# Kernel optimization log

Hardware: AMD Instinct MI355X
Metric: run time of the kernel (lower is better)

The kernel has to match this reference:

```python
import jax, jax.numpy as jnp
import numpy as np

VTH = 1.0
U_REST = -VTH          # default u_rest = -vth
DV = VTH - U_REST      # reset-subtract magnitude = 2.0
LEAKY = 0.9
FB_NUM = 1

B, D_IN, N, L, T = 16384, 512, 512, 3, 32
W_SCALE = 0.05


def _lif(u):
    # threshold-compare, reset-subtract, leaky-decay
    s = (u >= VTH).astype(u.dtype)
    u = (u - DV * s) * LEAKY
    return u, s


def setup_inputs() -> dict:
    key = jax.random.key(0)
    k1, k2, k3 = jax.random.split(key, 3)
    x = jax.random.normal(k1, (B, D_IN), dtype=jnp.float32)
    Wx = jax.random.normal(k2, (N, D_IN), dtype=jnp.float32) * W_SCALE
    bx = jnp.zeros((N,), dtype=jnp.float32)
    Ws = jax.random.normal(k3, (L, N, N), dtype=jnp.float32) * W_SCALE
    bs = jnp.zeros((L, N), dtype=jnp.float32)
    return {"x": x, "Wx": Wx, "bx": bx, "Ws": Ws, "bs": bs, "time_step": T}


def reference(x, Wx, bx, Ws, bs, time_step):
    L_ = Ws.shape[0]
    x1 = x @ Wx.T + bx  # constant input current, [B, N]

    # ---- first timestep: initialize all layers sequentially ----
    u0, s0 = _lif(x1)
    us, ss = [u0], [s0]
    for i in range(L_ - 1):
        ui, si = _lif(ss[-1] @ Ws[i].T + bs[i])
        us.append(ui)
        ss.append(si)
    u = jnp.stack(us)  # [L, B, N]
    s = jnp.stack(ss)
    a = s              # leaky-weighted spike accumulator

    # ---- remaining time_step-1 steps ----
    def step(carry, _):
        u, s, a = carry
        new_u, new_s = [], []
        # first layer gets feedback from last layer's spikes + constant input
        u0 = u[0] + s[L_ - 1] @ Ws[L_ - 1].T + bs[L_ - 1] + x1
        u0n, s0n = _lif(u0)
        new_u.append(u0n)
        new_s.append(s0n)
        # subsequent layers use the spikes just produced this timestep
        for i in range(L_ - 1):
            ui = u[i + 1] + new_s[i] @ Ws[i].T + bs[i]
            uin, sin_ = _lif(ui)
            new_u.append(uin)
            new_s.append(sin_)
        u = jnp.stack(new_u)
        s = jnp.stack(new_s)
        a = a * LEAKY + s
        return (u, s, a), None

    (u, s, a), _ = jax.lax.scan(step, (u, s, a), None, length=time_step - 1)

    weighted = (1.0 - LEAKY ** time_step) / (1.0 - LEAKY)
    a = a / weighted
    # f_type='all', fb_num=1 -> (a_list[0], a_list[-1])
    return a[0], a[L_ - 1]
```

## Files before the change

### kernel.cpp

```cpp
#include <hip/hip_runtime.h>
#include <stdint.h>


#define B_SZ 16384
#define N_SZ 512
#define K_SZ 512
#define T_STEPS 32
#define LEAKY 0.9f

#define CHUNK 16

__device__ inline uint32_t spread4(uint32_t b) {
    b = (b | (b << 12)) & 0x000F000Fu;
    b = (b | (b << 6))  & 0x03030303u;
    b = (b | (b << 3))  & 0x11111111u;
    return b;
}

__device__ inline uint32_t mask_word8(const unsigned long long bal[8], int lane) {
    const uint32_t sh = (4u * (uint32_t)lane) & 31u;
    uint32_t word = 0;
    #pragma unroll
    for (int j = 0; j < 8; ++j) {
        const uint32_t half = (lane < 8) ? (uint32_t)bal[j] : (uint32_t)(bal[j] >> 32);
        const uint32_t nib  = (half >> sh) & 0xFu;
        word |= ((nib * 0x00204081u) & 0x01010101u) << j;
    }
    return word;
}

template<int AMODE, bool ADD_U, bool ADD_X1>
__global__ __launch_bounds__(1024, 1)
void spgemm_lif(const uint32_t* __restrict__ mIn,
                const float* __restrict__ Wt,
                const float* __restrict__ bias,
                const float* u_prev,
                const float* __restrict__ x1,
                float* u_out,
                uint32_t* __restrict__ mOut,
                float* a_ptr)
{
    __shared__ float Wl[2][CHUNK * 512];

    const int tid  = threadIdx.x;
    const int lane = tid & 63;
    const int w    = tid >> 6;
    const int rg   = w >> 1;
    const int g    = w & 1;
    const int r0   = blockIdx.x * 64 + rg * 8;
    const int cb   = g * 256 + lane * 4;

    float acc[8][4];
    #pragma unroll
    for (int m = 0; m < 8; ++m)
        #pragma unroll
        for (int j = 0; j < 4; ++j) acc[m][j] = 0.f;

    auto stage = [&](int c, int bf) {
        const float* src = Wt + (size_t)c * (CHUNK * 512);
        #pragma unroll
        for (int i = 0; i < 2; ++i) {
            const int seg = w * 2 + i;
            __builtin_amdgcn_global_load_lds(
                (const __attribute__((address_space(1))) unsigned int*)
                    (src + seg * 256 + lane * 4),
                (__attribute__((address_space(3))) unsigned int*)
                    (&Wl[bf][seg * 256]),
                16, 0, 0);
        }
    };

    auto compute = [&](int bf, const uint32_t* msr, int sh) {
        const float* base = &Wl[bf][0];
        #pragma unroll
        for (int m = 0; m < 8; ++m) {
            uint32_t wrd = (msr[m] >> sh) & 0xFFFFu;
            while (wrd) {
                const int kk = __builtin_ctz(wrd);
                wrd &= wrd - 1u;
                const float4 wv = *(const float4*)(base + kk * 512 + cb);
                acc[m][0] += wv.x;
                acc[m][1] += wv.y;
                acc[m][2] += wv.z;
                acc[m][3] += wv.w;
            }
        }
    };

    uint32_t mv = mIn[r0 + (lane & 7)];
    stage(0, 0);
    __syncthreads();

    int cur = 0;
    uint32_t msr[8];
    for (int c = 0; c < 32; ++c) {
        if (c + 1 < 32) stage(c + 1, cur ^ 1);
        if ((c & 1) == 0) {
            #pragma unroll
            for (int m = 0; m < 8; ++m)
                msr[m] = __builtin_amdgcn_readlane(mv, m);
            const int pn = (c >> 1) + 1;
            if (pn < 16) mv = mIn[(size_t)pn * B_SZ + r0 + (lane & 7)];
        }
        compute(cur, msr, (c & 1) * 16);
        __syncthreads();
        cur ^= 1;
    }

    const float4 bv = *(const float4*)(bias + cb);
    const int msel = lane & 7;
    unsigned long long balsel[4] = {0ull, 0ull, 0ull, 0ull};

    #pragma unroll
    for (int m = 0; m < 8; ++m) {
        const size_t row = (size_t)(r0 + m) * N_SZ + cb;
        float v[4];
        v[0] = acc[m][0] + bv.x; v[1] = acc[m][1] + bv.y;
        v[2] = acc[m][2] + bv.z; v[3] = acc[m][3] + bv.w;
        if (ADD_U) {
            const float4 ua = *(const float4*)(u_prev + row);
            v[0] += ua.x; v[1] += ua.y; v[2] += ua.z; v[3] += ua.w;
        }
        if (ADD_X1) {
            const float4 xa = *(const float4*)(x1 + row);
            v[0] += xa.x; v[1] += xa.y; v[2] += xa.z; v[3] += xa.w;
        }
        float un[4], sv[4];
        #pragma unroll
        for (int j = 0; j < 4; ++j) {
            sv[j] = (v[j] >= 1.0f) ? 1.0f : 0.0f;
            un[j] = (v[j] - 2.0f * sv[j]) * LEAKY;
        }
        *(float4*)(u_out + row) = (float4){un[0], un[1], un[2], un[3]};
        if (AMODE == 1) {
            *(float4*)(a_ptr + row) = (float4){sv[0], sv[1], sv[2], sv[3]};
        } else if (AMODE == 2) {
            const float4 aa = *(const float4*)(a_ptr + row);
            *(float4*)(a_ptr + row) = (float4){aa.x * LEAKY + sv[0], aa.y * LEAKY + sv[1],
                                               aa.z * LEAKY + sv[2], aa.w * LEAKY + sv[3]};
        }
        unsigned long long bal[4];
        #pragma unroll
        for (int j = 0; j < 4; ++j) bal[j] = __ballot(v[j] >= 1.0f);
        #pragma unroll
        for (int j = 0; j < 4; ++j)
            balsel[j] = (m == msel) ? bal[j] : balsel[j];
    }

    const int h = lane >> 3;
    uint32_t pk = 0;
    #pragma unroll
    for (int j = 0; j < 4; ++j)
        pk |= spread4((uint32_t)(balsel[j] >> (8 * h)) & 0xFFu) << j;
    mOut[(size_t)(g * 8 + h) * B_SZ + r0 + msel] = pk;
}

__global__ void mask_build(const uint16_t* __restrict__ s, uint32_t* __restrict__ mOut) {
    const int lane = threadIdx.x & 63;
    const int w    = threadIdx.x >> 6;
    const int r0   = blockIdx.x * 32 + w * 8;
    const int cb   = lane * 8;
    uint32_t pk[8];
    #pragma unroll
    for (int m = 0; m < 8; ++m) {
        const ushort4 sa = ((const ushort4*)(s + (size_t)(r0 + m) * N_SZ + cb))[0];
        const ushort4 sb = ((const ushort4*)(s + (size_t)(r0 + m) * N_SZ + cb))[1];
        const uint16_t sv[8] = {sa.x, sa.y, sa.z, sa.w, sb.x, sb.y, sb.z, sb.w};
        unsigned long long bal[8];
        #pragma unroll
        for (int j = 0; j < 8; ++j) bal[j] = __ballot(sv[j] != 0);
        pk[m] = mask_word8(bal, lane);
    }
    if (lane < 16) {
        uint32_t* mp = mOut + (size_t)lane * B_SZ + r0;
        ((uint4*)mp)[0] = (uint4){pk[0], pk[1], pk[2], pk[3]};
        ((uint4*)mp)[1] = (uint4){pk[4], pk[5], pk[6], pk[7]};
    }
}

#define BM 128
#define BN 128
#define BK 16
#define TM 8
#define TN 8
#define PAD 4

__global__ __launch_bounds__(256, 2)
void gemm0_lif(const float* __restrict__ A, const float* __restrict__ W,
               const float* __restrict__ bias, float* __restrict__ u_out,
               uint16_t* __restrict__ s_out, float* __restrict__ a_ptr,
               float* __restrict__ c_out) {
    __shared__ float As[BK][BM + PAD];
    __shared__ float Bs[BK][BN + PAD];
    const int tid = threadIdx.x;
    const int tx = tid & 15, ty = tid >> 4;
    const int m0 = blockIdx.y * BM, n0 = blockIdx.x * BN;
    float acc[TM][TN];
    #pragma unroll
    for (int i = 0; i < TM; ++i)
        #pragma unroll
        for (int j = 0; j < TN; ++j) acc[i][j] = 0.f;
    const int lr = tid >> 2, lc = (tid & 3) * 4;
    for (int k0 = 0; k0 < K_SZ; k0 += BK) {
        #pragma unroll
        for (int h = 0; h < 2; ++h) {
            const int r = lr + h * 64;
            const float4 v = *(const float4*)(A + (size_t)(m0 + r) * K_SZ + k0 + lc);
            As[lc + 0][r] = v.x; As[lc + 1][r] = v.y;
            As[lc + 2][r] = v.z; As[lc + 3][r] = v.w;
        }
        #pragma unroll
        for (int h = 0; h < 2; ++h) {
            const int r = lr + h * 64;
            const float4 v = *(const float4*)(W + (size_t)(n0 + r) * K_SZ + k0 + lc);
            Bs[lc + 0][r] = v.x; Bs[lc + 1][r] = v.y;
            Bs[lc + 2][r] = v.z; Bs[lc + 3][r] = v.w;
        }
        __syncthreads();
        #pragma unroll
        for (int kk = 0; kk < BK; ++kk) {
            float av[TM], bvv[TN];
            #pragma unroll
            for (int i = 0; i < TM; ++i) av[i] = As[kk][ty * TM + i];
            #pragma unroll
            for (int j = 0; j < TN; ++j) bvv[j] = Bs[kk][tx * TN + j];
            #pragma unroll
            for (int i = 0; i < TM; ++i)
                #pragma unroll
                for (int j = 0; j < TN; ++j)
                    acc[i][j] = fmaf(av[i], bvv[j], acc[i][j]);
        }
        __syncthreads();
    }
    #pragma unroll
    for (int i = 0; i < TM; ++i) {
        const size_t row = (size_t)(m0 + ty * TM + i) * N_SZ + n0 + tx * TN;
        #pragma unroll
        for (int j = 0; j < TN; ++j) {
            const float v = acc[i][j] + bias[n0 + tx * TN + j];
            c_out[row + j] = v;
            const float sv = (v >= 1.0f) ? 1.0f : 0.0f;
            u_out[row + j] = (v - 2.0f * sv) * LEAKY;
            s_out[row + j] = (v >= 1.0f) ? (uint16_t)0x3F80 : (uint16_t)0;
            a_ptr[row + j] = sv;
        }
    }
}

__global__ void transpose512(const float* __restrict__ in, float* __restrict__ out) {
    __shared__ float t[32][33];
    const int mat = blockIdx.z;
    const int bx = blockIdx.x * 32, by = blockIdx.y * 32;
    const int x = threadIdx.x & 31, yg = threadIdx.x >> 5;
    const float* I = in + (size_t)mat * N_SZ * K_SZ;
    float* O = out + (size_t)mat * N_SZ * K_SZ;
    #pragma unroll
    for (int i = 0; i < 4; ++i)
        t[yg * 4 + i][x] = I[(size_t)(by + yg * 4 + i) * 512 + bx + x];
    __syncthreads();
    #pragma unroll
    for (int i = 0; i < 4; ++i)
        O[(size_t)(bx + yg * 4 + i) * 512 + by + x] = t[x][yg * 4 + i];
}

__global__ void scale_kernel(float* __restrict__ p, float inv, int n4) {
    int i = blockIdx.x * blockDim.x + threadIdx.x;
    const int stride = gridDim.x * blockDim.x;
    for (; i < n4; i += stride) {
        float4 v = ((float4*)p)[i];
        v.x *= inv; v.y *= inv; v.z *= inv; v.w *= inv;
        ((float4*)p)[i] = v;
    }
}

extern "C" void kernel_launch(void* const* d_in, const int* in_sizes, int n_in,
                              void* d_out, int out_size, void* d_ws, size_t ws_size,
                              hipStream_t stream) {
    const float* x  = (const float*)d_in[0];
    const float* Wx = (const float*)d_in[1];
    const float* bx = (const float*)d_in[2];
    const float* Ws = (const float*)d_in[3];
    const float* bs = (const float*)d_in[4];

    const size_t BNt = (size_t)B_SZ * N_SZ;
    const size_t NK  = (size_t)N_SZ * K_SZ;
    const size_t MSZ = (size_t)16 * B_SZ;

    float*    u   = (float*)d_ws;
    float*    x1  = u + 3 * BNt;
    uint16_t* s0b = (uint16_t*)(x1 + BNt);
    float*    WsT = (float*)(s0b + BNt);
    uint32_t* mT  = (uint32_t*)(WsT + 3 * NK + 4096);
    uint32_t* mT0 = mT;
    uint32_t* mT1 = mT + MSZ;
    uint32_t* mT2 = mT + 2 * MSZ;

    float* a0 = (float*)d_out;
    float* a2 = a0 + BNt;
    float* u0 = u; float* u1 = u + BNt; float* u2 = u + 2 * BNt;

    dim3 blkS(1024);
    dim3 blk(256);
    dim3 gridV(N_SZ / BN, B_SZ / BM);
    dim3 gridS(B_SZ / 64);
    dim3 gridM(B_SZ / 32);
    dim3 gridT(16, 16, 3);

    transpose512<<<gridT, blk, 0, stream>>>(Ws, WsT);

    gemm0_lif<<<gridV, blk, 0, stream>>>(x, Wx, bx, u0, s0b, a0, x1);
    mask_build<<<gridM, blk, 0, stream>>>(s0b, mT0);
    spgemm_lif<0, false, false><<<gridS, blkS, 0, stream>>>(
        mT0, WsT, bs, nullptr, nullptr, u1, mT1, nullptr);
    spgemm_lif<1, false, false><<<gridS, blkS, 0, stream>>>(
        mT1, WsT + NK, bs + N_SZ, nullptr, nullptr, u2, mT2, a2);

    for (int t = 1; t < T_STEPS; ++t) {
        spgemm_lif<2, true, true><<<gridS, blkS, 0, stream>>>(
            mT2, WsT + 2 * NK, bs + 2 * N_SZ, u0, x1, u0, mT0, a0);
        spgemm_lif<0, true, false><<<gridS, blkS, 0, stream>>>(
            mT0, WsT, bs, u1, nullptr, u1, mT1, nullptr);
        spgemm_lif<2, true, false><<<gridS, blkS, 0, stream>>>(
            mT1, WsT + NK, bs + N_SZ, u2, nullptr, u2, mT2, a2);
    }

    double p = 1.0;
    for (int i = 0; i < T_STEPS; ++i) p *= 0.9;
    const float inv = (float)(1.0 / ((1.0 - p) / 0.1));
    scale_kernel<<<2048, blk, 0, stream>>>((float*)d_out, inv, (int)(2 * BNt / 4));
}
```

Measured before the change: 6.365 ms.

## Split spike GEMM block into sparse LDS waves and dense FMA waves

Each 64-row block now runs 12 waves instead of 16. Eight waves handle the first 32 rows with the existing sparse, mask-driven accumulation from double-buffered LDS weight chunks. Four waves handle the other 32 rows with a dense, branch-free FMA loop that reads weights straight from global memory. Launch bounds change to 768 threads with two blocks per CU, aiming to overlap LDS-bound and VALU-bound work and to raise occupancy. The risk is that the dense half does the full K work regardless of spike sparsity and is tied to the sparse waves through shared barriers, so it may end up limiting the block.

```diff
diff --git a/kernel.cpp b/kernel.cpp
--- a/kernel.cpp
+++ b/kernel.cpp
@@ -30,8 +30,8 @@
 }
 
 template<int AMODE, bool ADD_U, bool ADD_X1>
-__global__ __launch_bounds__(1024, 1)
-void spgemm_lif(const uint32_t* __restrict__ mIn,
+__global__ __launch_bounds__(768, 2)
+void hybrid_lif(const uint32_t* __restrict__ mIn,
                 const float* __restrict__ Wt,
                 const float* __restrict__ bias,
                 const float* u_prev,
@@ -45,114 +45,236 @@
     const int tid  = threadIdx.x;
     const int lane = tid & 63;
     const int w    = tid >> 6;
-    const int rg   = w >> 1;
-    const int g    = w & 1;
-    const int r0   = blockIdx.x * 64 + rg * 8;
-    const int cb   = g * 256 + lane * 4;
-
-    float acc[8][4];
-    #pragma unroll
-    for (int m = 0; m < 8; ++m)
-        #pragma unroll
-        for (int j = 0; j < 4; ++j) acc[m][j] = 0.f;
-
-    auto stage = [&](int c, int bf) {
-        const float* src = Wt + (size_t)c * (CHUNK * 512);
-        #pragma unroll
-        for (int i = 0; i < 2; ++i) {
-            const int seg = w * 2 + i;
-            __builtin_amdgcn_global_load_lds(
-                (const __attribute__((address_space(1))) unsigned int*)
-                    (src + seg * 256 + lane * 4),
-                (__attribute__((address_space(3))) unsigned int*)
-                    (&Wl[bf][seg * 256]),
-                16, 0, 0);
-        }
-    };
-
-    auto compute = [&](int bf, const uint32_t* msr, int sh) {
-        const float* base = &Wl[bf][0];
+
+    if (w < 8) {
+        const int rg = w >> 1;
+        const int g  = w & 1;
+        const int r0 = blockIdx.x * 64 + rg * 8;
+        const int cb = g * 256 + lane * 4;
+
+        float acc[8][4];
+        #pragma unroll
+        for (int m = 0; m < 8; ++m)
+            #pragma unroll
+            for (int j = 0; j < 4; ++j) acc[m][j] = 0.f;
+
+        auto stage = [&](int c, int bf) {
+            const float* src = Wt + (size_t)c * (CHUNK * 512);
+            #pragma unroll
+            for (int i = 0; i < 4; ++i) {
+                const int seg = w * 4 + i;
+                __builtin_amdgcn_global_load_lds(
+                    (const __attribute__((address_space(1))) unsigned int*)
+                        (src + seg * 256 + lane * 4),
+                    (__attribute__((address_space(3))) unsigned int*)
+                        (&Wl[bf][seg * 256]),
+                    16, 0, 0);
+            }
+        };
+
+        auto compute = [&](int bf, const uint32_t* msr, int sh) {
+            const float* base = &Wl[bf][0];
+            #pragma unroll
+            for (int m = 0; m < 8; ++m) {
+                uint32_t wrd = (msr[m] >> sh) & 0xFFFFu;
+                while (wrd) {
+                    const int kk = __builtin_ctz(wrd);
+                    wrd &= wrd - 1u;
+                    const float4 wv = *(const float4*)(base + kk * 512 + cb);
+                    acc[m][0] += wv.x;
+                    acc[m][1] += wv.y;
+                    acc[m][2] += wv.z;
+                    acc[m][3] += wv.w;
+                }
+            }
+        };
+
+        uint32_t mv = mIn[r0 + (lane & 7)];
+        stage(0, 0);
+        __syncthreads();
+
+        int cur = 0;
+        uint32_t msr[8];
+        for (int c = 0; c < 32; ++c) {
+            if (c + 1 < 32) stage(c + 1, cur ^ 1);
+            if ((c & 1) == 0) {
+                #pragma unroll
+                for (int m = 0; m < 8; ++m)
+                    msr[m] = __builtin_amdgcn_readlane(mv, m);
+                const int pn = (c >> 1) + 1;
+                if (pn < 16) mv = mIn[(size_t)pn * B_SZ + r0 + (lane & 7)];
+            }
+            compute(cur, msr, (c & 1) * 16);
+            __syncthreads();
+            cur ^= 1;
+        }
+
+        const float4 bv = *(const float4*)(bias + cb);
+        const int msel = lane & 7;
+        unsigned long long balsel[4] = {0ull, 0ull, 0ull, 0ull};
+
         #pragma unroll
         for (int m = 0; m < 8; ++m) {
-            uint32_t wrd = (msr[m] >> sh) & 0xFFFFu;
-            while (wrd) {
-                const int kk = __builtin_ctz(wrd);
-                wrd &= wrd - 1u;
-                const float4 wv = *(const float4*)(base + kk * 512 + cb);
-                acc[m][0] += wv.x;
-                acc[m][1] += wv.y;
-                acc[m][2] += wv.z;
-                acc[m][3] += wv.w;
-            }
-        }
-    };
-
-    uint32_t mv = mIn[r0 + (lane & 7)];
-    stage(0, 0);
-    __syncthreads();
-
-    int cur = 0;
-    uint32_t msr[8];
-    for (int c = 0; c < 32; ++c) {
-        if (c + 1 < 32) stage(c + 1, cur ^ 1);
-        if ((c & 1) == 0) {
-            #pragma unroll
-            for (int m = 0; m < 8; ++m)
-                msr[m] = __builtin_amdgcn_readlane(mv, m);
-            const int pn = (c >> 1) + 1;
-            if (pn < 16) mv = mIn[(size_t)pn * B_SZ + r0 + (lane & 7)];
-        }
-        compute(cur, msr, (c & 1) * 16);
+            const size_t row = (size_t)(r0 + m) * N_SZ + cb;
+            float v[4];
+            v[0] = acc[m][0] + bv.x; v[1] = acc[m][1] + bv.y;
+            v[2] = acc[m][2] + bv.z; v[3] = acc[m][3] + bv.w;
+            if (ADD_U) {
+                const float4 ua = *(const float4*)(u_prev + row);
+                v[0] += ua.x; v[1] += ua.y; v[2] += ua.z; v[3] += ua.w;
+            }
+            if (ADD_X1) {
+                const float4 xa = *(const float4*)(x1 + row);
+                v[0] += xa.x; v[1] += xa.y; v[2] += xa.z; v[3] += xa.w;
+            }
+            float un[4], sv[4];
+            #pragma unroll
+            for (int j = 0; j < 4; ++j) {
+                sv[j] = (v[j] >= 1.0f) ? 1.0f : 0.0f;
+                un[j] = (v[j] - 2.0f * sv[j]) * LEAKY;
+            }
+            *(float4*)(u_out + row) = (float4){un[0], un[1], un[2], un[3]};
+            if (AMODE == 1) {
+                *(float4*)(a_ptr + row) = (float4){sv[0], sv[1], sv[2], sv[3]};
+            } else if (AMODE == 2) {
+                const float4 aa = *(const float4*)(a_ptr + row);
+                *(float4*)(a_ptr + row) = (float4){aa.x * LEAKY + sv[0], aa.y * LEAKY + sv[1],
+                                                   aa.z * LEAKY + sv[2], aa.w * LEAKY + sv[3]};
+            }
+            unsigned long long bal[4];
+            #pragma unroll
+            for (int j = 0; j < 4; ++j) bal[j] = __ballot(v[j] >= 1.0f);
+            #pragma unroll
+            for (int j = 0; j < 4; ++j)
+                balsel[j] = (m == msel) ? bal[j] : balsel[j];
+        }
+
+        const int h = lane >> 3;
+        uint32_t pk = 0;
+        #pragma unroll
+        for (int j = 0; j < 4; ++j)
+            pk |= spread4((uint32_t)(balsel[j] >> (8 * h)) & 0xFFu) << j;
+        mOut[(size_t)(g * 8 + h) * B_SZ + r0 + msel] = pk;
+
+    } else {
+        const int r0 = blockIdx.x * 64 + 32 + (w - 8) * 8;
+        const int cb = lane * 8;
+
+        float acc[8][8];
+        #pragma unroll
+        for (int m = 0; m < 8; ++m)
+            #pragma unroll
+            for (int j = 0; j < 8; ++j) acc[m][j] = 0.f;
+
+        const float* wb = Wt + cb;
+        float4 w0a = ((const float4*)wb)[0];
+        float4 w0b = ((const float4*)wb)[1];
+        float4 w1a = ((const float4*)(wb + 512))[0];
+        float4 w1b = ((const float4*)(wb + 512))[1];
+
+        uint32_t mv = mIn[r0 + (lane & 7)];
         __syncthreads();
-        cur ^= 1;
-    }
-
-    const float4 bv = *(const float4*)(bias + cb);
-    const int msel = lane & 7;
-    unsigned long long balsel[4] = {0ull, 0ull, 0ull, 0ull};
-
-    #pragma unroll
-    for (int m = 0; m < 8; ++m) {
-        const size_t row = (size_t)(r0 + m) * N_SZ + cb;
-        float v[4];
-        v[0] = acc[m][0] + bv.x; v[1] = acc[m][1] + bv.y;
-        v[2] = acc[m][2] + bv.z; v[3] = acc[m][3] + bv.w;
-        if (ADD_U) {
-            const float4 ua = *(const float4*)(u_prev + row);
-            v[0] += ua.x; v[1] += ua.y; v[2] += ua.z; v[3] += ua.w;
-        }
-        if (ADD_X1) {
-            const float4 xa = *(const float4*)(x1 + row);
-            v[0] += xa.x; v[1] += xa.y; v[2] += xa.z; v[3] += xa.w;
-        }
-        float un[4], sv[4];
-        #pragma unroll
-        for (int j = 0; j < 4; ++j) {
-            sv[j] = (v[j] >= 1.0f) ? 1.0f : 0.0f;
-            un[j] = (v[j] - 2.0f * sv[j]) * LEAKY;
-        }
-        *(float4*)(u_out + row) = (float4){un[0], un[1], un[2], un[3]};
-        if (AMODE == 1) {
-            *(float4*)(a_ptr + row) = (float4){sv[0], sv[1], sv[2], sv[3]};
-        } else if (AMODE == 2) {
-            const float4 aa = *(const float4*)(a_ptr + row);
-            *(float4*)(a_ptr + row) = (float4){aa.x * LEAKY + sv[0], aa.y * LEAKY + sv[1],
-                                               aa.z * LEAKY + sv[2], aa.w * LEAKY + sv[3]};
-        }
-        unsigned long long bal[4];
-        #pragma unroll
-        for (int j = 0; j < 4; ++j) bal[j] = __ballot(v[j] >= 1.0f);
-        #pragma unroll
-        for (int j = 0; j < 4; ++j)
-            balsel[j] = (m == msel) ? bal[j] : balsel[j];
-    }
-
-    const int h = lane >> 3;
-    uint32_t pk = 0;
-    #pragma unroll
-    for (int j = 0; j < 4; ++j)
-        pk |= spread4((uint32_t)(balsel[j] >> (8 * h)) & 0xFFu) << j;
-    mOut[(size_t)(g * 8 + h) * B_SZ + r0 + msel] = pk;
+
+        uint32_t ms[8];
+        for (int c = 0; c < 32; ++c) {
+            if ((c & 1) == 0) {
+                #pragma unroll
+                for (int m = 0; m < 8; ++m)
+                    ms[m] = __builtin_amdgcn_readlane(mv, m);
+                const int pn = (c >> 1) + 1;
+                if (pn < 16) mv = mIn[(size_t)pn * B_SZ + r0 + (lane & 7)];
+            }
+            const int sh = (c & 1) * 16;
+            #pragma unroll
+            for (int kp = 0; kp < 8; ++kp) {
+                const int k = c * 16 + 2 * kp;
+                const float* pf = wb + (size_t)(k + 2) * 512;
+                const float4 n0a = ((const float4*)pf)[0];
+                const float4 n0b = ((const float4*)pf)[1];
+                const float4 n1a = ((const float4*)(pf + 512))[0];
+                const float4 n1b = ((const float4*)(pf + 512))[1];
+                #pragma unroll
+                for (int m = 0; m < 8; ++m) {
+                    const float sm = ((ms[m] >> (sh + 2 * kp)) & 1u) ? 1.0f : 0.0f;
+                    acc[m][0] = fmaf(sm, w0a.x, acc[m][0]);
+                    acc[m][1] = fmaf(sm, w0a.y, acc[m][1]);
+                    acc[m][2] = fmaf(sm, w0a.z, acc[m][2]);
+                    acc[m][3] = fmaf(sm, w0a.w, acc[m][3]);
+                    acc[m][4] = fmaf(sm, w0b.x, acc[m][4]);
+                    acc[m][5] = fmaf(sm, w0b.y, acc[m][5]);
+                    acc[m][6] = fmaf(sm, w0b.z, acc[m][6]);
+                    acc[m][7] = fmaf(sm, w0b.w, acc[m][7]);
+                }
+                #pragma unroll
+                for (int m = 0; m < 8; ++m) {
+                    const float sm = ((ms[m] >> (sh + 2 * kp + 1)) & 1u) ? 1.0f : 0.0f;
+                    acc[m][0] = fmaf(sm, w1a.x, acc[m][0]);
+                    acc[m][1] = fmaf(sm, w1a.y, acc[m][1]);
+                    acc[m][2] = fmaf(sm, w1a.z, acc[m][2]);
+                    acc[m][3] = fmaf(sm, w1a.w, acc[m][3]);
+                    acc[m][4] = fmaf(sm, w1b.x, acc[m][4]);
+                    acc[m][5] = fmaf(sm, w1b.y, acc[m][5]);
+                    acc[m][6] = fmaf(sm, w1b.z, acc[m][6]);
+                    acc[m][7] = fmaf(sm, w1b.w, acc[m][7]);
+                }
+                w0a = n0a; w0b = n0b; w1a = n1a; w1b = n1b;
+            }
+            __syncthreads();
+        }
+
+        float4 bva = ((const float4*)(bias + cb))[0];
+        float4 bvb = ((const float4*)(bias + cb))[1];
+        float bv[8] = {bva.x, bva.y, bva.z, bva.w, bvb.x, bvb.y, bvb.z, bvb.w};
+
+        uint32_t pk[8];
+        #pragma unroll
+        for (int m = 0; m < 8; ++m) {
+            const size_t row = (size_t)(r0 + m) * N_SZ + cb;
+            float v[8];
+            #pragma unroll
+            for (int j = 0; j < 8; ++j) v[j] = acc[m][j] + bv[j];
+            if (ADD_U) {
+                const float4 ua = ((const float4*)(u_prev + row))[0];
+                const float4 ub = ((const float4*)(u_prev + row))[1];
+                v[0] += ua.x; v[1] += ua.y; v[2] += ua.z; v[3] += ua.w;
+                v[4] += ub.x; v[5] += ub.y; v[6] += ub.z; v[7] += ub.w;
+            }
+            if (ADD_X1) {
+                const float4 xa = ((const float4*)(x1 + row))[0];
+                const float4 xb = ((const float4*)(x1 + row))[1];
+                v[0] += xa.x; v[1] += xa.y; v[2] += xa.z; v[3] += xa.w;
+                v[4] += xb.x; v[5] += xb.y; v[6] += xb.z; v[7] += xb.w;
+            }
+            float un[8], sv[8];
+            #pragma unroll
+            for (int j = 0; j < 8; ++j) {
+                sv[j] = (v[j] >= 1.0f) ? 1.0f : 0.0f;
+                un[j] = (v[j] - 2.0f * sv[j]) * LEAKY;
+            }
+            ((float4*)(u_out + row))[0] = (float4){un[0], un[1], un[2], un[3]};
+            ((float4*)(u_out + row))[1] = (float4){un[4], un[5], un[6], un[7]};
+            if (AMODE == 1) {
+                ((float4*)(a_ptr + row))[0] = (float4){sv[0], sv[1], sv[2], sv[3]};
+                ((float4*)(a_ptr + row))[1] = (float4){sv[4], sv[5], sv[6], sv[7]};
+            } else if (AMODE == 2) {
+                const float4 aa = ((const float4*)(a_ptr + row))[0];
+                const float4 ab = ((const float4*)(a_ptr + row))[1];
+                ((float4*)(a_ptr + row))[0] = (float4){aa.x * LEAKY + sv[0], aa.y * LEAKY + sv[1],
+                                                       aa.z * LEAKY + sv[2], aa.w * LEAKY + sv[3]};
+                ((float4*)(a_ptr + row))[1] = (float4){ab.x * LEAKY + sv[4], ab.y * LEAKY + sv[5],
+                                                       ab.z * LEAKY + sv[6], ab.w * LEAKY + sv[7]};
+            }
+            unsigned long long bal[8];
+            #pragma unroll
+            for (int j = 0; j < 8; ++j) bal[j] = __ballot(v[j] >= 1.0f);
+            pk[m] = mask_word8(bal, lane);
+        }
+        if (lane < 16) {
+            uint32_t* mp = mOut + (size_t)lane * B_SZ + r0;
+            ((uint4*)mp)[0] = (uint4){pk[0], pk[1], pk[2], pk[3]};
+            ((uint4*)mp)[1] = (uint4){pk[4], pk[5], pk[6], pk[7]};
+        }
+    }
 }
 
 __global__ void mask_build(const uint16_t* __restrict__ s, uint32_t* __restrict__ mOut) {
@@ -299,10 +421,10 @@
     float* a2 = a0 + BNt;
     float* u0 = u; float* u1 = u + BNt; float* u2 = u + 2 * BNt;
 
-    dim3 blkS(1024);
+    dim3 blkH(768);
     dim3 blk(256);
     dim3 gridV(N_SZ / BN, B_SZ / BM);
-    dim3 gridS(B_SZ / 64);
+    dim3 gridH(B_SZ / 64);
     dim3 gridM(B_SZ / 32);
     dim3 gridT(16, 16, 3);
 
@@ -310,17 +432,17 @@
 
     gemm0_lif<<<gridV, blk, 0, stream>>>(x, Wx, bx, u0, s0b, a0, x1);
     mask_build<<<gridM, blk, 0, stream>>>(s0b, mT0);
-    spgemm_lif<0, false, false><<<gridS, blkS, 0, stream>>>(
+    hybrid_lif<0, false, false><<<gridH, blkH, 0, stream>>>(
         mT0, WsT, bs, nullptr, nullptr, u1, mT1, nullptr);
-    spgemm_lif<1, false, false><<<gridS, blkS, 0, stream>>>(
+    hybrid_lif<1, false, false><<<gridH, blkH, 0, stream>>>(
         mT1, WsT + NK, bs + N_SZ, nullptr, nullptr, u2, mT2, a2);
 
     for (int t = 1; t < T_STEPS; ++t) {
-        spgemm_lif<2, true, true><<<gridS, blkS, 0, stream>>>(
+        hybrid_lif<2, true, true><<<gridH, blkH, 0, stream>>>(
             mT2, WsT + 2 * NK, bs + 2 * N_SZ, u0, x1, u0, mT0, a0);
-        spgemm_lif<0, true, false><<<gridS, blkS, 0, stream>>>(
+        hybrid_lif<0, true, false><<<gridH, blkH, 0, stream>>>(
             mT0, WsT, bs, u1, nullptr, u1, mT1, nullptr);
-        spgemm_lif<2, true, false><<<gridS, blkS, 0, stream>>>(
+        hybrid_lif<2, true, false><<<gridH, blkH, 0, stream>>>(
             mT1, WsT + NK, bs + N_SZ, u2, nullptr, u2, mT2, a2);
     }
 
```

Measured after the change: 10.39 ms. +63.2%, slower.

## Split spiking GEMM columns between LDS-staged and direct global weight reads

Applied to the files above, without the earlier changes.

Each wave now owns 4 rows and all 512 output columns. The first 256 weight columns come from a half-size double-buffered LDS chunk and the other 256 are read directly from global memory (likely L2-resident). The block shrinks to 512 threads with launch bounds asking for 4 blocks per CU, and the grid doubles. The sparse accumulation loop is software-pipelined so the next gather is issued before the current one is accumulated, aiming to hide load latency and raise occupancy. The cost is divergent, uncoalesced global gathers for half the columns, higher register pressure from the doubled accumulators, and more complex mask packing.

```diff
diff --git a/kernel.cpp b/kernel.cpp
--- a/kernel.cpp
+++ b/kernel.cpp
@@ -30,7 +30,7 @@
 }
 
 template<int AMODE, bool ADD_U, bool ADD_X1>
-__global__ __launch_bounds__(1024, 1)
+__global__ __launch_bounds__(512, 4)
 void spgemm_lif(const uint32_t* __restrict__ mIn,
                 const float* __restrict__ Wt,
                 const float* __restrict__ bias,
@@ -40,119 +40,160 @@
                 uint32_t* __restrict__ mOut,
                 float* a_ptr)
 {
-    __shared__ float Wl[2][CHUNK * 512];
+    __shared__ float Wl[2][CHUNK * 256];
 
     const int tid  = threadIdx.x;
     const int lane = tid & 63;
     const int w    = tid >> 6;
-    const int rg   = w >> 1;
-    const int g    = w & 1;
-    const int r0   = blockIdx.x * 64 + rg * 8;
-    const int cb   = g * 256 + lane * 4;
-
-    float acc[8][4];
-    #pragma unroll
-    for (int m = 0; m < 8; ++m)
-        #pragma unroll
-        for (int j = 0; j < 4; ++j) acc[m][j] = 0.f;
+    const int r0   = blockIdx.x * 32 + w * 4;
+    const int cl   = lane * 4;
+    const int cg   = 256 + lane * 4;
+
+    float acc[4][8];
+    #pragma unroll
+    for (int m = 0; m < 4; ++m)
+        #pragma unroll
+        for (int j = 0; j < 8; ++j) acc[m][j] = 0.f;
 
     auto stage = [&](int c, int bf) {
-        const float* src = Wt + (size_t)c * (CHUNK * 512);
         #pragma unroll
         for (int i = 0; i < 2; ++i) {
             const int seg = w * 2 + i;
+            const float* src = Wt + (size_t)(c * CHUNK + seg) * 512 + lane * 4;
             __builtin_amdgcn_global_load_lds(
-                (const __attribute__((address_space(1))) unsigned int*)
-                    (src + seg * 256 + lane * 4),
-                (__attribute__((address_space(3))) unsigned int*)
-                    (&Wl[bf][seg * 256]),
+                (const __attribute__((address_space(1))) unsigned int*)src,
+                (__attribute__((address_space(3))) unsigned int*)(&Wl[bf][seg * 256]),
                 16, 0, 0);
         }
     };
 
-    auto compute = [&](int bf, const uint32_t* msr, int sh) {
+    auto compute = [&](int bf, const uint32_t* msr, int sh, const float* Wg) {
         const float* base = &Wl[bf][0];
-        #pragma unroll
-        for (int m = 0; m < 8; ++m) {
-            uint32_t wrd = (msr[m] >> sh) & 0xFFFFu;
-            while (wrd) {
-                const int kk = __builtin_ctz(wrd);
-                wrd &= wrd - 1u;
-                const float4 wv = *(const float4*)(base + kk * 512 + cb);
-                acc[m][0] += wv.x;
-                acc[m][1] += wv.y;
-                acc[m][2] += wv.z;
-                acc[m][3] += wv.w;
+        uint32_t wrd[4];
+        float4 lq[4], gq[4];
+        int pend = 0;
+        #pragma unroll
+        for (int m = 0; m < 4; ++m) {
+            wrd[m] = (msr[m] >> sh) & 0xFFFFu;
+            if (wrd[m]) {
+                const int k = __builtin_ctz(wrd[m]);
+                wrd[m] &= wrd[m] - 1u;
+                lq[m] = *(const float4*)(base + k * 256 + cl);
+                gq[m] = *(const float4*)(Wg + (size_t)k * 512 + cg);
+                pend |= (1 << m);
             }
         }
+        while (pend) {
+            #pragma unroll
+            for (int m = 0; m < 4; ++m) {
+                if (pend & (1 << m)) {
+                    const float4 lv = lq[m];
+                    const float4 gv = gq[m];
+                    if (wrd[m]) {
+                        const int k = __builtin_ctz(wrd[m]);
+                        wrd[m] &= wrd[m] - 1u;
+                        lq[m] = *(const float4*)(base + k * 256 + cl);
+                        gq[m] = *(const float4*)(Wg + (size_t)k * 512 + cg);
+                    } else {
+                        pend &= ~(1 << m);
+                    }
+                    acc[m][0] += lv.x; acc[m][1] += lv.y;
+                    acc[m][2] += lv.z; acc[m][3] += lv.w;
+                    acc[m][4] += gv.x; acc[m][5] += gv.y;
+                    acc[m][6] += gv.z; acc[m][7] += gv.w;
+                }
+            }
+        }
     };
 
-    uint32_t mv = mIn[r0 + (lane & 7)];
+    uint32_t mv = mIn[r0 + (lane & 3)];
     stage(0, 0);
     __syncthreads();
 
     int cur = 0;
-    uint32_t msr[8];
+    uint32_t msr[4];
     for (int c = 0; c < 32; ++c) {
         if (c + 1 < 32) stage(c + 1, cur ^ 1);
         if ((c & 1) == 0) {
             #pragma unroll
-            for (int m = 0; m < 8; ++m)
+            for (int m = 0; m < 4; ++m)
                 msr[m] = __builtin_amdgcn_readlane(mv, m);
             const int pn = (c >> 1) + 1;
-            if (pn < 16) mv = mIn[(size_t)pn * B_SZ + r0 + (lane & 7)];
-        }
-        compute(cur, msr, (c & 1) * 16);
+            if (pn < 16) mv = mIn[(size_t)pn * B_SZ + r0 + (lane & 3)];
+        }
+        compute(cur, msr, (c & 1) * 16, Wt + (size_t)(c * CHUNK) * 512);
         __syncthreads();
         cur ^= 1;
     }
 
-    const float4 bv = *(const float4*)(bias + cb);
-    const int msel = lane & 7;
-    unsigned long long balsel[4] = {0ull, 0ull, 0ull, 0ull};
-
-    #pragma unroll
-    for (int m = 0; m < 8; ++m) {
-        const size_t row = (size_t)(r0 + m) * N_SZ + cb;
-        float v[4];
-        v[0] = acc[m][0] + bv.x; v[1] = acc[m][1] + bv.y;
-        v[2] = acc[m][2] + bv.z; v[3] = acc[m][3] + bv.w;
+    const float4 bva = *(const float4*)(bias + cl);
+    const float4 bvb = *(const float4*)(bias + cg);
+    const int msel = lane & 3;
+    unsigned long long balL[4] = {0ull, 0ull, 0ull, 0ull};
+    unsigned long long balG[4] = {0ull, 0ull, 0ull, 0ull};
+
+    #pragma unroll
+    for (int m = 0; m < 4; ++m) {
+        const size_t rowL = (size_t)(r0 + m) * N_SZ + cl;
+        const size_t rowG = (size_t)(r0 + m) * N_SZ + cg;
+        float v[8];
+        v[0] = acc[m][0] + bva.x; v[1] = acc[m][1] + bva.y;
+        v[2] = acc[m][2] + bva.z; v[3] = acc[m][3] + bva.w;
+        v[4] = acc[m][4] + bvb.x; v[5] = acc[m][5] + bvb.y;
+        v[6] = acc[m][6] + bvb.z; v[7] = acc[m][7] + bvb.w;
         if (ADD_U) {
-            const float4 ua = *(const float4*)(u_prev + row);
+            const float4 ua = *(const float4*)(u_prev + rowL);
+            const float4 ub = *(const float4*)(u_prev + rowG);
             v[0] += ua.x; v[1] += ua.y; v[2] += ua.z; v[3] += ua.w;
+            v[4] += ub.x; v[5] += ub.y; v[6] += ub.z; v[7] += ub.w;
         }
         if (ADD_X1) {
-            const float4 xa = *(const float4*)(x1 + row);
+            const float4 xa = *(const float4*)(x1 + rowL);
+            const float4 xb = *(const float4*)(x1 + rowG);
             v[0] += xa.x; v[1] += xa.y; v[2] += xa.z; v[3] += xa.w;
-        }
-        float un[4], sv[4];
-        #pragma unroll
-        for (int j = 0; j < 4; ++j) {
+            v[4] += xb.x; v[5] += xb.y; v[6] += xb.z; v[7] += xb.w;
+        }
+        float un[8], sv[8];
+        #pragma unroll
+        for (int j = 0; j < 8; ++j) {
             sv[j] = (v[j] >= 1.0f) ? 1.0f : 0.0f;
             un[j] = (v[j] - 2.0f * sv[j]) * LEAKY;
         }
-        *(float4*)(u_out + row) = (float4){un[0], un[1], un[2], un[3]};
+        *(float4*)(u_out + rowL) = (float4){un[0], un[1], un[2], un[3]};
+        *(float4*)(u_out + rowG) = (float4){un[4], un[5], un[6], un[7]};
         if (AMODE == 1) {
-            *(float4*)(a_ptr + row) = (float4){sv[0], sv[1], sv[2], sv[3]};
+            *(float4*)(a_ptr + rowL) = (float4){sv[0], sv[1], sv[2], sv[3]};
+            *(float4*)(a_ptr + rowG) = (float4){sv[4], sv[5], sv[6], sv[7]};
         } else if (AMODE == 2) {
-            const float4 aa = *(const float4*)(a_ptr + row);
-            *(float4*)(a_ptr + row) = (float4){aa.x * LEAKY + sv[0], aa.y * LEAKY + sv[1],
-                                               aa.z * LEAKY + sv[2], aa.w * LEAKY + sv[3]};
-        }
-        unsigned long long bal[4];
-        #pragma unroll
-        for (int j = 0; j < 4; ++j) bal[j] = __ballot(v[j] >= 1.0f);
-        #pragma unroll
-        for (int j = 0; j < 4; ++j)
-            balsel[j] = (m == msel) ? bal[j] : balsel[j];
-    }
-
-    const int h = lane >> 3;
+            const float4 aa = *(const float4*)(a_ptr + rowL);
+            const float4 ab = *(const float4*)(a_ptr + rowG);
+            *(float4*)(a_ptr + rowL) = (float4){aa.x * LEAKY + sv[0], aa.y * LEAKY + sv[1],
+                                                aa.z * LEAKY + sv[2], aa.w * LEAKY + sv[3]};
+            *(float4*)(a_ptr + rowG) = (float4){ab.x * LEAKY + sv[4], ab.y * LEAKY + sv[5],
+                                                ab.z * LEAKY + sv[6], ab.w * LEAKY + sv[7]};
+        }
+        unsigned long long bl[4], bg[4];
+        #pragma unroll
+        for (int j = 0; j < 4; ++j) bl[j] = __ballot(v[j] >= 1.0f);
+        #pragma unroll
+        for (int j = 0; j < 4; ++j) bg[j] = __ballot(v[4 + j] >= 1.0f);
+        #pragma unroll
+        for (int j = 0; j < 4; ++j) {
+            balL[j] = (m == msel) ? bl[j] : balL[j];
+            balG[j] = (m == msel) ? bg[j] : balG[j];
+        }
+    }
+
+    const int pidx = lane >> 2;
+    const int pp   = pidx & 7;
+    const bool gh  = pidx >= 8;
     uint32_t pk = 0;
     #pragma unroll
-    for (int j = 0; j < 4; ++j)
-        pk |= spread4((uint32_t)(balsel[j] >> (8 * h)) & 0xFFu) << j;
-    mOut[(size_t)(g * 8 + h) * B_SZ + r0 + msel] = pk;
+    for (int j = 0; j < 4; ++j) {
+        const unsigned long long b = gh ? balG[j] : balL[j];
+        pk |= spread4((uint32_t)(b >> (8 * pp)) & 0xFFu) << j;
+    }
+    mOut[(size_t)pidx * B_SZ + r0 + msel] = pk;
 }
 
 __global__ void mask_build(const uint16_t* __restrict__ s, uint32_t* __restrict__ mOut) {
@@ -299,10 +340,10 @@
     float* a2 = a0 + BNt;
     float* u0 = u; float* u1 = u + BNt; float* u2 = u + 2 * BNt;
 
-    dim3 blkS(1024);
+    dim3 blkS(512);
     dim3 blk(256);
     dim3 gridV(N_SZ / BN, B_SZ / BM);
-    dim3 gridS(B_SZ / 64);
+    dim3 gridS(B_SZ / 32);
     dim3 gridM(B_SZ / 32);
     dim3 gridT(16, 16, 3);
 
```

After: 8.531 ms. 1.34x slower.
